# Kernel tuning notes

Hardware: AMD Instinct MI355X
Metric: run time of the kernel (lower is better)

Reference implementation:

```python
import jax, jax.numpy as jnp
import numpy as np

N_NODES = 100000

def setup_inputs() -> dict:
    key = jax.random.key(0)
    k1, k2, k3 = jax.random.split(key, 3)
    x = jax.random.normal(k1, (N_NODES, 64), dtype=jnp.float32)
    edge_index = jax.random.randint(k2, (2, 1250000), 0, N_NODES, dtype=jnp.int64)
    edge_weight = jax.random.uniform(k3, (1250000,), dtype=jnp.float32)
    return {"x": x, "edge_index": edge_index, "edge_weight": edge_weight}

def reference(x, edge_index, edge_weight):
    # LightGCNConv: out[dst] = sum_e edge_weight[e] * x[src_e]  (aggr='add')
    src, dst = edge_index[0], edge_index[1]
    msgs = edge_weight[:, None] * x[src]          # [E, d] gather-multiply
    out = jax.ops.segment_sum(msgs, dst, num_segments=N_NODES)  # scatter-add
    return out
```

## Files before the change

### kernel.cpp

```cpp
#include <hip/hip_runtime.h>
#include <hip/hip_bf16.h>


#define N_NODES   100000
#define N_FEAT    64

#define A_BSH     7
#define A_NPB     (1 << A_BSH)
#define A_KB      ((N_NODES + A_NPB - 1) >> A_BSH)
#define A_CAP     2048
#define A_FCHUNK  8192
#define A_OVCAP   65536
#define NBIN      ((1250000 + A_FCHUNK - 1) / A_FCHUNK)
#define NCAST     391

__global__ __launch_bounds__(1024) void k_castbin(
    const float* __restrict__ x, ushort* __restrict__ xb,
    const int* __restrict__ ei, const float* __restrict__ w,
    int* __restrict__ bcur, int2* __restrict__ stg,
    int* __restrict__ ovf, int* __restrict__ ovcnt, int E) {
    int t = threadIdx.x;
    if (blockIdx.x >= NBIN) {
        int cb = blockIdx.x - NBIN;
        #pragma unroll
        for (int k = 0; k < 4; ++k) {
            int i4 = cb * 4096 + k * 1024 + t;
            if (i4 < N_NODES * N_FEAT / 4) {
                float4 v = ((const float4*)x)[i4];
                uint4 u = *(uint4*)&v;
                ushort4 r;
                r.x = (ushort)((u.x + 0x7FFFu + ((u.x >> 16) & 1)) >> 16);
                r.y = (ushort)((u.y + 0x7FFFu + ((u.y >> 16) & 1)) >> 16);
                r.z = (ushort)((u.z + 0x7FFFu + ((u.z >> 16) & 1)) >> 16);
                r.w = (ushort)((u.w + 0x7FFFu + ((u.w >> 16) & 1)) >> 16);
                ((ushort4*)xb)[i4] = r;
            }
        }
        return;
    }
    __shared__ int h[A_KB];
    for (int b = t; b < A_KB; b += 1024) h[b] = 0;
    __syncthreads();
    int e0 = blockIdx.x * A_FCHUNK;
    #pragma unroll
    for (int k = 0; k < A_FCHUNK / 1024; ++k) {
        int e = e0 + k * 1024 + t;
        if (e < E) atomicAdd(&h[ei[E + e] >> A_BSH], 1);
    }
    __syncthreads();
    for (int b = t; b < A_KB; b += 1024) {
        int c = h[b];
        h[b] = c ? atomicAdd(&bcur[b], c) : 0;
    }
    __syncthreads();
    #pragma unroll
    for (int k = 0; k < A_FCHUNK / 1024; ++k) {
        int e = e0 + k * 1024 + t;
        if (e < E) {
            int dst = ei[E + e];
            int b = dst >> A_BSH;
            int loc = atomicAdd(&h[b], 1);
            if (loc < A_CAP) {
                stg[b * A_CAP + loc] =
                    make_int2(ei[e] | ((dst & (A_NPB - 1)) << 17),
                              __float_as_int(w[e]));
            } else {
                int oi = atomicAdd(ovcnt, 1);
                if (oi < A_OVCAP) ovf[oi] = e;
            }
        }
    }
}

__global__ __launch_bounds__(256) void k_sort(
    int2* __restrict__ stg, const int* __restrict__ bcur,
    int* __restrict__ beg, int* __restrict__ endp) {
    __shared__ int2 buf[A_CAP];
    __shared__ int  hist[A_NPB];
    __shared__ int  cur[A_NPB];
    __shared__ int  sdata[256];
    int b = blockIdx.x, t = threadIdx.x;
    int cnt = bcur[b];
    if (cnt > A_CAP) cnt = A_CAP;
    int base = b * A_CAP;

    if (t < A_NPB) hist[t] = 0;
    __syncthreads();
    for (int i = t; i < cnt; i += 256) {
        int2 p = stg[base + i];
        buf[i] = p;
        atomicAdd(&hist[(p.x >> 17) & (A_NPB - 1)], 1);
    }
    __syncthreads();
    int c = (t < A_NPB) ? hist[t] : 0;
    sdata[t] = c; __syncthreads();
    for (int off = 1; off < 256; off <<= 1) {
        int v = (t >= off) ? sdata[t - off] : 0;
        __syncthreads();
        if (t >= off) sdata[t] += v;
        __syncthreads();
    }
    int excl = (t == 0) ? 0 : sdata[t - 1];
    if (t < A_NPB) {
        cur[t] = excl;
        int node = (b << A_BSH) + t;
        if (node < N_NODES) { beg[node] = base + excl; endp[node] = base + excl + c; }
    }
    __syncthreads();
    for (int i = t; i < cnt; i += 256) {
        int2 p = buf[i];
        int pos = atomicAdd(&cur[(p.x >> 17) & (A_NPB - 1)], 1);
        stg[base + pos] = p;
    }
}

__global__ __launch_bounds__(256) void k_gather4(
    const ushort* __restrict__ xb, const int* __restrict__ beg,
    const int* __restrict__ endp, const int2* __restrict__ stg,
    float* __restrict__ out) {
    int wid  = threadIdx.x >> 6;
    int lane = threadIdx.x & 63;
    int q    = lane >> 4;
    int l    = lane & 15;
    int node = blockIdx.x * 16 + wid * 4 + q;
    if (node >= N_NODES) return;
    int j = beg[node], end = endp[node];
    const ushort4* xb4 = (const ushort4*)xb;
    float ax0 = 0.f, ay0 = 0.f, az0 = 0.f, aw0 = 0.f;
    float ax1 = 0.f, ay1 = 0.f, az1 = 0.f, aw1 = 0.f;
    for (; j + 1 < end; j += 2) {
        int2 p0 = stg[j];
        int2 p1 = stg[j + 1];
        ushort4 u0 = xb4[(size_t)(p0.x & 0x1FFFF) * 16 + l];
        ushort4 u1 = xb4[(size_t)(p1.x & 0x1FFFF) * 16 + l];
        float w0 = __int_as_float(p0.y), w1 = __int_as_float(p1.y);
        ax0 += w0 * __uint_as_float((uint)u0.x << 16);
        ay0 += w0 * __uint_as_float((uint)u0.y << 16);
        az0 += w0 * __uint_as_float((uint)u0.z << 16);
        aw0 += w0 * __uint_as_float((uint)u0.w << 16);
        ax1 += w1 * __uint_as_float((uint)u1.x << 16);
        ay1 += w1 * __uint_as_float((uint)u1.y << 16);
        az1 += w1 * __uint_as_float((uint)u1.z << 16);
        aw1 += w1 * __uint_as_float((uint)u1.w << 16);
    }
    if (j < end) {
        int2 p = stg[j];
        ushort4 u = xb4[(size_t)(p.x & 0x1FFFF) * 16 + l];
        float wv = __int_as_float(p.y);
        ax0 += wv * __uint_as_float((uint)u.x << 16);
        ay0 += wv * __uint_as_float((uint)u.y << 16);
        az0 += wv * __uint_as_float((uint)u.z << 16);
        aw0 += wv * __uint_as_float((uint)u.w << 16);
    }
    float4 r;
    r.x = ax0 + ax1; r.y = ay0 + ay1; r.z = az0 + az1; r.w = aw0 + aw1;
    ((float4*)out)[(size_t)node * 16 + l] = r;
}

__global__ __launch_bounds__(256) void k_ovf(
    const float* __restrict__ x, const int* __restrict__ ei,
    const float* __restrict__ w, const int* __restrict__ ovf,
    const int* __restrict__ ovcnt, float* __restrict__ out, int E) {
    int n = *ovcnt;
    if (n > A_OVCAP) n = A_OVCAP;
    int wid  = blockIdx.x * 4 + (threadIdx.x >> 6);
    int lane = threadIdx.x & 63;
    for (int i = wid; i < n; i += gridDim.x * 4) {
        int e = ovf[i];
        float v = w[e] * x[(size_t)ei[e] * N_FEAT + lane];
        atomicAdd(&out[(size_t)ei[E + e] * N_FEAT + lane], v);
    }
}

#define BSH       8
#define NPB       (1 << BSH)
#define KB        ((N_NODES + NPB - 1) >> BSH)
#define FCHUNK    8192
#define SORT_CAP  4096

__global__ __launch_bounds__(256) void k_chist(
    const int* __restrict__ ei, int* __restrict__ bcur, int E) {
    __shared__ int h[KB];
    int t = threadIdx.x;
    for (int b = t; b < KB; b += 256) h[b] = 0;
    __syncthreads();
    int e0 = blockIdx.x * FCHUNK;
    #pragma unroll
    for (int k = 0; k < FCHUNK / 256; ++k) {
        int e = e0 + k * 256 + t;
        if (e < E) atomicAdd(&h[ei[E + e] >> BSH], 1);
    }
    __syncthreads();
    for (int b = t; b < KB; b += 256) if (h[b]) atomicAdd(&bcur[b], h[b]);
}

__global__ __launch_bounds__(256) void k_cscan(
    int* __restrict__ bcur, int* __restrict__ boffs) {
    __shared__ int sdata[256];
    int t = threadIdx.x;
    int i0 = 2 * t, i1 = 2 * t + 1;
    int v0 = (i0 < KB) ? bcur[i0] : 0;
    int v1 = (i1 < KB) ? bcur[i1] : 0;
    sdata[t] = v0 + v1; __syncthreads();
    for (int off = 1; off < 256; off <<= 1) {
        int v = (t >= off) ? sdata[t - off] : 0;
        __syncthreads();
        if (t >= off) sdata[t] += v;
        __syncthreads();
    }
    int run = (t == 0) ? 0 : sdata[t - 1];
    if (i0 < KB) { boffs[i0] = run; bcur[i0] = run; }
    run += v0;
    if (i1 < KB) { boffs[i1] = run; bcur[i1] = run; }
    if (t == 255) boffs[KB] = sdata[255];
}

__global__ __launch_bounds__(256) void k_cbin(
    const int* __restrict__ ei, const float* __restrict__ w,
    int* __restrict__ bcur, int2* __restrict__ stg, int E) {
    __shared__ int h[KB];
    int t = threadIdx.x;
    for (int b = t; b < KB; b += 256) h[b] = 0;
    __syncthreads();
    int e0 = blockIdx.x * FCHUNK;
    #pragma unroll
    for (int k = 0; k < FCHUNK / 256; ++k) {
        int e = e0 + k * 256 + t;
        if (e < E) atomicAdd(&h[ei[E + e] >> BSH], 1);
    }
    __syncthreads();
    for (int b = t; b < KB; b += 256) {
        int c = h[b];
        h[b] = c ? atomicAdd(&bcur[b], c) : 0;
    }
    __syncthreads();
    #pragma unroll
    for (int k = 0; k < FCHUNK / 256; ++k) {
        int e = e0 + k * 256 + t;
        if (e < E) {
            int dst = ei[E + e];
            int slot = atomicAdd(&h[dst >> BSH], 1);
            stg[slot] = make_int2(ei[e] | ((dst & (NPB - 1)) << 17),
                                  __float_as_int(w[e]));
        }
    }
}

__global__ __launch_bounds__(256) void k_csort(
    int2* __restrict__ stg, const int* __restrict__ boffs,
    int* __restrict__ offs) {
    __shared__ int2 buf[SORT_CAP];
    __shared__ int  hist[NPB];
    __shared__ int  cur[NPB];
    __shared__ int  sdata[256];
    int b = blockIdx.x, t = threadIdx.x;
    int bg = boffs[b], end = boffs[b + 1], cnt = end - bg;
    for (int n = t; n < NPB; n += 256) hist[n] = 0;
    __syncthreads();
    int nlds = cnt < SORT_CAP ? cnt : SORT_CAP;
    for (int i = t; i < nlds; i += 256) {
        int2 p = stg[bg + i];
        buf[i] = p;
        atomicAdd(&hist[(p.x >> 17) & (NPB - 1)], 1);
    }
    int2 r0{0,0}, r1{0,0}; int nr = 0;
    {
        int i0 = nlds + t, i1 = nlds + 256 + t;
        if (i0 < cnt) { r0 = stg[bg + i0]; atomicAdd(&hist[(r0.x >> 17) & (NPB - 1)], 1); nr = 1; }
        if (i1 < cnt) { r1 = stg[bg + i1]; atomicAdd(&hist[(r1.x >> 17) & (NPB - 1)], 1); nr = 2; }
    }
    __syncthreads();
    int c = hist[t];
    sdata[t] = c; __syncthreads();
    for (int off = 1; off < 256; off <<= 1) {
        int v = (t >= off) ? sdata[t - off] : 0;
        __syncthreads();
        if (t >= off) sdata[t] += v;
        __syncthreads();
    }
    int excl = (t == 0) ? 0 : sdata[t - 1];
    cur[t] = excl;
    int node = (b << BSH) + t;
    if (node < N_NODES) offs[node] = bg + excl;
    if (b == KB - 1 && t == 255) offs[N_NODES] = end;
    __syncthreads();
    for (int i = t; i < nlds; i += 256) {
        int2 p = buf[i];
        int pos = atomicAdd(&cur[(p.x >> 17) & (NPB - 1)], 1);
        stg[bg + pos] = p;
    }
    if (nr >= 1) { int pos = atomicAdd(&cur[(r0.x >> 17) & (NPB - 1)], 1); stg[bg + pos] = r0; }
    if (nr >= 2) { int pos = atomicAdd(&cur[(r1.x >> 17) & (NPB - 1)], 1); stg[bg + pos] = r1; }
}

__global__ __launch_bounds__(256) void k_gather(
    const float* __restrict__ x, const int* __restrict__ offs,
    const int2* __restrict__ stg, float* __restrict__ out) {
    int node = blockIdx.x * 4 + (threadIdx.x >> 6);
    int lane = threadIdx.x & 63;
    if (node >= N_NODES) return;
    int bg = offs[node], end = offs[node + 1];
    float a0 = 0.f, a1 = 0.f, a2 = 0.f, a3 = 0.f;
    int j = bg;
    for (; j + 3 < end; j += 4) {
        int2 p0 = stg[j];
        int2 p1 = stg[j + 1];
        int2 p2 = stg[j + 2];
        int2 p3 = stg[j + 3];
        a0 += __int_as_float(p0.y) * x[(size_t)(p0.x & 0x1FFFF) * N_FEAT + lane];
        a1 += __int_as_float(p1.y) * x[(size_t)(p1.x & 0x1FFFF) * N_FEAT + lane];
        a2 += __int_as_float(p2.y) * x[(size_t)(p2.x & 0x1FFFF) * N_FEAT + lane];
        a3 += __int_as_float(p3.y) * x[(size_t)(p3.x & 0x1FFFF) * N_FEAT + lane];
    }
    for (; j < end; ++j) {
        int2 p = stg[j];
        a0 += __int_as_float(p.y) * x[(size_t)(p.x & 0x1FFFF) * N_FEAT + lane];
    }
    out[(size_t)node * N_FEAT + lane] = (a0 + a1) + (a2 + a3);
}

__global__ __launch_bounds__(256) void gnn_scatter_kernel(
    const float* __restrict__ x, const int* __restrict__ ei,
    const float* __restrict__ w, float* __restrict__ out, int E) {
    int e = blockIdx.x * 4 + (threadIdx.x >> 6);
    int lane = threadIdx.x & 63;
    if (e >= E) return;
    float v = w[e] * x[(size_t)ei[e] * N_FEAT + lane];
    atomicAdd(&out[(size_t)ei[E + e] * N_FEAT + lane], v);
}

static inline size_t align16(size_t v) { return (v + 15) & ~(size_t)15; }

extern "C" void kernel_launch(void* const* d_in, const int* in_sizes, int n_in,
                              void* d_out, int out_size, void* d_ws, size_t ws_size,
                              hipStream_t stream) {
    const float* x   = (const float*)d_in[0];
    const int*   ei  = (const int*)d_in[1];
    const float* w   = (const float*)d_in[2];
    float*       out = (float*)d_out;
    const int E = in_sizes[2];
    char* ws = (char*)d_ws;

    size_t a_xb   = 0;
    size_t a_stg  = align16(a_xb + (size_t)N_NODES * N_FEAT * 2);
    size_t a_beg  = align16(a_stg + (size_t)A_KB * A_CAP * 8);
    size_t a_end  = align16(a_beg + (size_t)N_NODES * 4);
    size_t a_bcur = align16(a_end + (size_t)N_NODES * 4);
    size_t a_ovf  = align16(a_bcur + (size_t)(A_KB + 1) * 4);
    size_t need_a = a_ovf + (size_t)A_OVCAP * 4;

    if (ws_size >= need_a && E == 1250000) {
        ushort* xb   = (ushort*)(ws + a_xb);
        int2*   stg  = (int2*)(ws + a_stg);
        int*    beg  = (int*)(ws + a_beg);
        int*    endp = (int*)(ws + a_end);
        int*    bcur = (int*)(ws + a_bcur);
        int*    ovcnt = bcur + A_KB;
        int*    ovf  = (int*)(ws + a_ovf);

        hipMemsetAsync(bcur, 0, (size_t)(A_KB + 1) * 4, stream);
        k_castbin<<<NBIN + NCAST, 1024, 0, stream>>>(
            x, xb, ei, w, bcur, stg, ovf, ovcnt, E);
        k_sort<<<A_KB, 256, 0, stream>>>(stg, bcur, beg, endp);
        k_gather4<<<(N_NODES + 15) / 16, 256, 0, stream>>>(xb, beg, endp, stg, out);
        k_ovf<<<16, 256, 0, stream>>>(x, ei, w, ovf, ovcnt, out, E);
        return;
    }

    size_t b_bcur  = 0;
    size_t b_boffs = align16(b_bcur + (size_t)KB * 4);
    size_t b_offs  = align16(b_boffs + (size_t)(KB + 1) * 4);
    size_t b_stg   = align16(b_offs + (size_t)(N_NODES + 1) * 4);
    size_t need_b  = b_stg + (size_t)E * 8;

    if (ws_size >= need_b) {
        int*  bcur  = (int*)(ws + b_bcur);
        int*  boffs = (int*)(ws + b_boffs);
        int*  offs  = (int*)(ws + b_offs);
        int2* stg   = (int2*)(ws + b_stg);
        const int nblk = (E + FCHUNK - 1) / FCHUNK;
        hipMemsetAsync(bcur, 0, (size_t)KB * 4, stream);
        k_chist<<<nblk, 256, 0, stream>>>(ei, bcur, E);
        k_cscan<<<1, 256, 0, stream>>>(bcur, boffs);
        k_cbin<<<nblk, 256, 0, stream>>>(ei, w, bcur, stg, E);
        k_csort<<<KB, 256, 0, stream>>>(stg, boffs, offs);
        k_gather<<<(N_NODES + 3) / 4, 256, 0, stream>>>(x, offs, stg, out);
        return;
    }

    hipMemsetAsync(d_out, 0, (size_t)out_size * sizeof(float), stream);
    gnn_scatter_kernel<<<(E + 3) / 4, 256, 0, stream>>>(x, ei, w, out, E);
}
```

Baseline: 158.4 us.

## Fuse bucket sort with gather and cache edge data in registers during binning

Merges the per-bucket sort kernel and the gather kernel into one 1024-thread kernel. The sorted edges stay in shared memory and are consumed directly, which removes the write-back of sorted staging data, the beg/end arrays and one launch. The binning kernel now keeps dst, src and weight in registers between its histogram pass and its scatter pass instead of reloading them, and halves the chunk size so there are more blocks. The cost is more shared memory per block and lower occupancy. Each wave now handles two passes of nodes, so per-bucket load imbalance may show up.

```diff
diff --git a/kernel.cpp b/kernel.cpp
--- a/kernel.cpp
+++ b/kernel.cpp
@@ -9,7 +9,7 @@
 #define A_NPB     (1 << A_BSH)
 #define A_KB      ((N_NODES + A_NPB - 1) >> A_BSH)
 #define A_CAP     2048
-#define A_FCHUNK  8192
+#define A_FCHUNK  4096
 #define A_OVCAP   65536
 #define NBIN      ((1250000 + A_FCHUNK - 1) / A_FCHUNK)
 #define NCAST     391
@@ -42,10 +42,17 @@
     for (int b = t; b < A_KB; b += 1024) h[b] = 0;
     __syncthreads();
     int e0 = blockIdx.x * A_FCHUNK;
+    int dstv[A_FCHUNK / 1024];
+    int srcv[A_FCHUNK / 1024];
+    float wv[A_FCHUNK / 1024];
     #pragma unroll
     for (int k = 0; k < A_FCHUNK / 1024; ++k) {
         int e = e0 + k * 1024 + t;
-        if (e < E) atomicAdd(&h[ei[E + e] >> A_BSH], 1);
+        bool ok = (e < E);
+        dstv[k] = ok ? ei[E + e] : -1;
+        srcv[k] = ok ? ei[e] : 0;
+        wv[k]   = ok ? w[e] : 0.f;
+        if (ok) atomicAdd(&h[dstv[k] >> A_BSH], 1);
     }
     __syncthreads();
     for (int b = t; b < A_KB; b += 1024) {
@@ -55,30 +62,29 @@
     __syncthreads();
     #pragma unroll
     for (int k = 0; k < A_FCHUNK / 1024; ++k) {
-        int e = e0 + k * 1024 + t;
-        if (e < E) {
-            int dst = ei[E + e];
-            int b = dst >> A_BSH;
+        if (dstv[k] >= 0) {
+            int b = dstv[k] >> A_BSH;
             int loc = atomicAdd(&h[b], 1);
             if (loc < A_CAP) {
                 stg[b * A_CAP + loc] =
-                    make_int2(ei[e] | ((dst & (A_NPB - 1)) << 17),
-                              __float_as_int(w[e]));
+                    make_int2(srcv[k] | ((dstv[k] & (A_NPB - 1)) << 17),
+                              __float_as_int(wv[k]));
             } else {
                 int oi = atomicAdd(ovcnt, 1);
-                if (oi < A_OVCAP) ovf[oi] = e;
+                if (oi < A_OVCAP) ovf[oi] = e0 + k * 1024 + t;
             }
         }
     }
 }
 
-__global__ __launch_bounds__(256) void k_sort(
-    int2* __restrict__ stg, const int* __restrict__ bcur,
-    int* __restrict__ beg, int* __restrict__ endp) {
+__global__ __launch_bounds__(1024) void k_sortgather(
+    const ushort* __restrict__ xb, const int* __restrict__ bcur,
+    const int2* __restrict__ stg, float* __restrict__ out) {
     __shared__ int2 buf[A_CAP];
+    __shared__ int2 srt[A_CAP];
     __shared__ int  hist[A_NPB];
+    __shared__ int  start[A_NPB];
     __shared__ int  cur[A_NPB];
-    __shared__ int  sdata[256];
     int b = blockIdx.x, t = threadIdx.x;
     int cnt = bcur[b];
     if (cnt > A_CAP) cnt = A_CAP;
@@ -86,75 +92,74 @@
 
     if (t < A_NPB) hist[t] = 0;
     __syncthreads();
-    for (int i = t; i < cnt; i += 256) {
+    for (int i = t; i < cnt; i += 1024) {
         int2 p = stg[base + i];
         buf[i] = p;
         atomicAdd(&hist[(p.x >> 17) & (A_NPB - 1)], 1);
     }
     __syncthreads();
-    int c = (t < A_NPB) ? hist[t] : 0;
-    sdata[t] = c; __syncthreads();
-    for (int off = 1; off < 256; off <<= 1) {
-        int v = (t >= off) ? sdata[t - off] : 0;
-        __syncthreads();
-        if (t >= off) sdata[t] += v;
-        __syncthreads();
-    }
-    int excl = (t == 0) ? 0 : sdata[t - 1];
-    if (t < A_NPB) {
-        cur[t] = excl;
-        int node = (b << A_BSH) + t;
-        if (node < N_NODES) { beg[node] = base + excl; endp[node] = base + excl + c; }
-    }
-    __syncthreads();
-    for (int i = t; i < cnt; i += 256) {
+    if (t < A_NPB) cur[t] = hist[t];
+    __syncthreads();
+    for (int off = 1; off < A_NPB; off <<= 1) {
+        int v = (t < A_NPB && t >= off) ? cur[t - off] : 0;
+        __syncthreads();
+        if (t < A_NPB && t >= off) cur[t] += v;
+        __syncthreads();
+    }
+    if (t < A_NPB) start[t] = (t == 0) ? 0 : cur[t - 1];
+    __syncthreads();
+    if (t < A_NPB) cur[t] = start[t];
+    __syncthreads();
+    for (int i = t; i < cnt; i += 1024) {
         int2 p = buf[i];
         int pos = atomicAdd(&cur[(p.x >> 17) & (A_NPB - 1)], 1);
-        stg[base + pos] = p;
-    }
-}
-
-__global__ __launch_bounds__(256) void k_gather4(
-    const ushort* __restrict__ xb, const int* __restrict__ beg,
-    const int* __restrict__ endp, const int2* __restrict__ stg,
-    float* __restrict__ out) {
-    int wid  = threadIdx.x >> 6;
-    int lane = threadIdx.x & 63;
+        srt[pos] = p;
+    }
+    __syncthreads();
+
+    int wid  = t >> 6;
+    int lane = t & 63;
     int q    = lane >> 4;
     int l    = lane & 15;
-    int node = blockIdx.x * 16 + wid * 4 + q;
-    if (node >= N_NODES) return;
-    int j = beg[node], end = endp[node];
     const ushort4* xb4 = (const ushort4*)xb;
-    float ax0 = 0.f, ay0 = 0.f, az0 = 0.f, aw0 = 0.f;
-    float ax1 = 0.f, ay1 = 0.f, az1 = 0.f, aw1 = 0.f;
-    for (; j + 1 < end; j += 2) {
-        int2 p0 = stg[j];
-        int2 p1 = stg[j + 1];
-        ushort4 u0 = xb4[(size_t)(p0.x & 0x1FFFF) * 16 + l];
-        ushort4 u1 = xb4[(size_t)(p1.x & 0x1FFFF) * 16 + l];
-        float w0 = __int_as_float(p0.y), w1 = __int_as_float(p1.y);
-        ax0 += w0 * __uint_as_float((uint)u0.x << 16);
-        ay0 += w0 * __uint_as_float((uint)u0.y << 16);
-        az0 += w0 * __uint_as_float((uint)u0.z << 16);
-        aw0 += w0 * __uint_as_float((uint)u0.w << 16);
-        ax1 += w1 * __uint_as_float((uint)u1.x << 16);
-        ay1 += w1 * __uint_as_float((uint)u1.y << 16);
-        az1 += w1 * __uint_as_float((uint)u1.z << 16);
-        aw1 += w1 * __uint_as_float((uint)u1.w << 16);
-    }
-    if (j < end) {
-        int2 p = stg[j];
-        ushort4 u = xb4[(size_t)(p.x & 0x1FFFF) * 16 + l];
-        float wv = __int_as_float(p.y);
-        ax0 += wv * __uint_as_float((uint)u.x << 16);
-        ay0 += wv * __uint_as_float((uint)u.y << 16);
-        az0 += wv * __uint_as_float((uint)u.z << 16);
-        aw0 += wv * __uint_as_float((uint)u.w << 16);
-    }
-    float4 r;
-    r.x = ax0 + ax1; r.y = ay0 + ay1; r.z = az0 + az1; r.w = aw0 + aw1;
-    ((float4*)out)[(size_t)node * 16 + l] = r;
+    #pragma unroll
+    for (int pass = 0; pass < 2; ++pass) {
+        int n = pass * 64 + wid * 4 + q;
+        int node = (b << A_BSH) + n;
+        int j = start[n], end = start[n] + hist[n];
+        float ax0 = 0.f, ay0 = 0.f, az0 = 0.f, aw0 = 0.f;
+        float ax1 = 0.f, ay1 = 0.f, az1 = 0.f, aw1 = 0.f;
+        for (; j + 1 < end; j += 2) {
+            int2 p0 = srt[j];
+            int2 p1 = srt[j + 1];
+            ushort4 u0 = xb4[(size_t)(p0.x & 0x1FFFF) * 16 + l];
+            ushort4 u1 = xb4[(size_t)(p1.x & 0x1FFFF) * 16 + l];
+            float w0 = __int_as_float(p0.y), w1 = __int_as_float(p1.y);
+            ax0 += w0 * __uint_as_float((uint)u0.x << 16);
+            ay0 += w0 * __uint_as_float((uint)u0.y << 16);
+            az0 += w0 * __uint_as_float((uint)u0.z << 16);
+            aw0 += w0 * __uint_as_float((uint)u0.w << 16);
+            ax1 += w1 * __uint_as_float((uint)u1.x << 16);
+            ay1 += w1 * __uint_as_float((uint)u1.y << 16);
+            az1 += w1 * __uint_as_float((uint)u1.z << 16);
+            aw1 += w1 * __uint_as_float((uint)u1.w << 16);
+        }
+        if (j < end) {
+            int2 p = srt[j];
+            ushort4 u = xb4[(size_t)(p.x & 0x1FFFF) * 16 + l];
+            float wv = __int_as_float(p.y);
+            ax0 += wv * __uint_as_float((uint)u.x << 16);
+            ay0 += wv * __uint_as_float((uint)u.y << 16);
+            az0 += wv * __uint_as_float((uint)u.z << 16);
+            aw0 += wv * __uint_as_float((uint)u.w << 16);
+        }
+        if (node < N_NODES) {
+            float4 r;
+            r.x = ax0 + ax1; r.y = ay0 + ay1;
+            r.z = az0 + az1; r.w = aw0 + aw1;
+            ((float4*)out)[(size_t)node * 16 + l] = r;
+        }
+    }
 }
 
 __global__ __launch_bounds__(256) void k_ovf(
@@ -343,26 +348,21 @@
 
     size_t a_xb   = 0;
     size_t a_stg  = align16(a_xb + (size_t)N_NODES * N_FEAT * 2);
-    size_t a_beg  = align16(a_stg + (size_t)A_KB * A_CAP * 8);
-    size_t a_end  = align16(a_beg + (size_t)N_NODES * 4);
-    size_t a_bcur = align16(a_end + (size_t)N_NODES * 4);
+    size_t a_bcur = align16(a_stg + (size_t)A_KB * A_CAP * 8);
     size_t a_ovf  = align16(a_bcur + (size_t)(A_KB + 1) * 4);
     size_t need_a = a_ovf + (size_t)A_OVCAP * 4;
 
     if (ws_size >= need_a && E == 1250000) {
-        ushort* xb   = (ushort*)(ws + a_xb);
-        int2*   stg  = (int2*)(ws + a_stg);
-        int*    beg  = (int*)(ws + a_beg);
-        int*    endp = (int*)(ws + a_end);
-        int*    bcur = (int*)(ws + a_bcur);
+        ushort* xb    = (ushort*)(ws + a_xb);
+        int2*   stg   = (int2*)(ws + a_stg);
+        int*    bcur  = (int*)(ws + a_bcur);
         int*    ovcnt = bcur + A_KB;
-        int*    ovf  = (int*)(ws + a_ovf);
+        int*    ovf   = (int*)(ws + a_ovf);
 
         hipMemsetAsync(bcur, 0, (size_t)(A_KB + 1) * 4, stream);
         k_castbin<<<NBIN + NCAST, 1024, 0, stream>>>(
             x, xb, ei, w, bcur, stg, ovf, ovcnt, E);
-        k_sort<<<A_KB, 256, 0, stream>>>(stg, bcur, beg, endp);
-        k_gather4<<<(N_NODES + 15) / 16, 256, 0, stream>>>(xb, beg, endp, stg, out);
+        k_sortgather<<<A_KB, 1024, 0, stream>>>(xb, bcur, stg, out);
         k_ovf<<<16, 256, 0, stream>>>(x, ei, w, ovf, ovcnt, out, E);
         return;
     }
```

Result: faster. 135.6 us (-14.4%).
